# Performance work log

Hardware: AMD Instinct MI355X
Metric: run time of the kernel (lower is better)

Reference implementation:

```python
import jax, jax.numpy as jnp
import numpy as np


def setup_inputs() -> dict:
    key = jax.random.key(0)
    ks = jax.random.split(key, 8)
    B, T, D, H, R = 64, 1024, 512, 512, 64
    s = lambda n: 1.0 / np.sqrt(n)
    return {
        "x":   jax.random.normal(ks[0], (B, T, D), jnp.float32),
        "W_w": jax.random.normal(ks[1], (4 * H, D), jnp.float32) * s(D),
        "W_b": jax.random.normal(ks[2], (4 * H,), jnp.float32) * 0.01,
        "U_w": jax.random.normal(ks[3], (4 * H, H), jnp.float32) * s(H),
        "U_b": jax.random.normal(ks[4], (4 * H,), jnp.float32) * 0.01,
        "A_w": jax.random.normal(ks[5], (R, D), jnp.float32) * s(D),
        "B_w": jax.random.normal(ks[6], (R, H), jnp.float32) * s(H),
        "P_w": jax.random.normal(ks[7], (H, R), jnp.float32) * s(R),
    }


def reference(x, W_w, W_b, U_w, U_b, A_w, B_w, P_w):
    # x: [B,T,D]. Dropout is identity (eval mode).
    Bsz, T, _ = x.shape
    H = U_w.shape[0] // 4
    # Precompute all input-side projections in parallel (no recurrence dep).
    Wx = jnp.einsum('btd,hd->bth', x, W_w) + W_b          # [B,T,4H]
    Ax = jnp.einsum('btd,rd->btr', x, A_w)                # [B,T,R]

    def step(carry, inp):
        h, c = carry
        wx_t, ax_t = inp                                  # [B,4H], [B,R]
        gates = wx_t + h @ U_w.T + U_b                    # [B,4H]
        i, f, o, g = jnp.split(gates, 4, axis=-1)
        i = jax.nn.sigmoid(i)
        f = jax.nn.sigmoid(f)
        o = jax.nn.sigmoid(o)
        g = jnp.tanh(g)
        mix = (ax_t * (h @ B_w.T)) @ P_w.T                # [B,H]
        c = f * c + i * g + 0.1 * mix
        h = o * jnp.tanh(c)
        return (h, c), h

    h0 = jnp.zeros((Bsz, H), x.dtype)
    c0 = jnp.zeros((Bsz, H), x.dtype)
    (h, c), outs = jax.lax.scan(
        step, (h0, c0),
        (jnp.swapaxes(Wx, 0, 1), jnp.swapaxes(Ax, 0, 1)))
    outs = jnp.swapaxes(outs, 0, 1)                       # [B,T,H]
    return outs, h, c
```

## Files before the change

### kernel.cpp

```cpp
#include <hip/hip_runtime.h>
#include <stdint.h>


typedef float    f32x4  __attribute__((ext_vector_type(4)));
typedef __bf16   bf16x8 __attribute__((ext_vector_type(8)));
typedef uint16_t u16;
typedef uint16_t u16x8  __attribute__((ext_vector_type(8)));

#define WS_XB     0
#define WS_WC     67108864
#define WS_BIAS   69337088
#define WS_U      69345792
#define WS_BW     71442944
#define WS_P      71508480
#define WS_HBUF   71574016
#define WS_CNT    71705088
#define WS_WXC    71706112

#define OUT_H     33554432
#define OUT_C     33587200

#define SMEM_BYTES (16384 + 4352 + 4352 + 1088)

__device__ __forceinline__ u16 f2bf(float f) {
  uint32_t u = __builtin_bit_cast(uint32_t, f);
  u = (u + 0x7fffu + ((u >> 16) & 1u)) >> 16;
  return (u16)u;
}
__device__ __forceinline__ float bf2f(u16 b) {
  uint32_t u = ((uint32_t)b) << 16;
  return __builtin_bit_cast(float, u);
}
__device__ __forceinline__ f32x4 mfma16(u16x8 a, u16x8 b, f32x4 c) {
  return __builtin_amdgcn_mfma_f32_16x16x32_bf16(
      __builtin_bit_cast(bf16x8, a), __builtin_bit_cast(bf16x8, b), c, 0, 0, 0);
}
__device__ __forceinline__ float sigm(float x) { return 1.f / (1.f + __expf(-x)); }
__device__ __forceinline__ float tanh_fast(float x) {
  float a = fabsf(x);
  float e = __expf(2.f * a);
  float t = 1.f - 2.f / (e + 1.f);
  return x < 0.f ? -t : t;
}

__global__ void cast_x(const float* __restrict__ x, u16* __restrict__ xb) {
  int i = blockIdx.x * 256 + threadIdx.x;
  const float4* src = (const float4*)x;
  float4 a = src[(size_t)i * 2];
  float4 b = src[(size_t)i * 2 + 1];
  u16x8 o;
  o[0] = f2bf(a.x); o[1] = f2bf(a.y); o[2] = f2bf(a.z); o[3] = f2bf(a.w);
  o[4] = f2bf(b.x); o[5] = f2bf(b.y); o[6] = f2bf(b.z); o[7] = f2bf(b.w);
  *(u16x8*)(xb + (size_t)i * 8) = o;
}

__global__ void prep(const float* __restrict__ W_w, const float* __restrict__ W_b,
                     const float* __restrict__ U_w, const float* __restrict__ U_b,
                     const float* __restrict__ A_w, const float* __restrict__ B_w,
                     const float* __restrict__ P_w,
                     u16* __restrict__ Wc, float* __restrict__ bias,
                     u16* __restrict__ Ubf, u16* __restrict__ Bwbf,
                     u16* __restrict__ Pbf, int* __restrict__ cnt) {
  const int total = 1114112 + 1048576 + 32768 + 32768 + 2176 + 256;
  for (int i = blockIdx.x * blockDim.x + threadIdx.x; i < total;
       i += gridDim.x * blockDim.x) {
    int idx = i;
    if (idx < 1114112) {
      int row = idx >> 9, k = idx & 511;
      float v = 0.f;
      if (row < 2048) v = W_w[row * 512 + k];
      else if (row < 2112) v = A_w[(row - 2048) * 512 + k];
      Wc[idx] = f2bf(v);
      continue;
    }
    idx -= 1114112;
    if (idx < 1048576) { Ubf[idx] = f2bf(U_w[idx]); continue; }
    idx -= 1048576;
    if (idx < 32768) { Bwbf[idx] = f2bf(B_w[idx]); continue; }
    idx -= 32768;
    if (idx < 32768) { Pbf[idx] = f2bf(0.1f * P_w[idx]); continue; }
    idx -= 32768;
    if (idx < 2176) {
      bias[idx] = (idx < 2048) ? (W_b[idx] + U_b[idx]) : 0.f;
      continue;
    }
    idx -= 2176;
    cnt[idx] = 0;
  }
}

__global__ void __launch_bounds__(256) gemm_wxc(const u16* __restrict__ xb,
                                                const u16* __restrict__ Wc,
                                                const float* __restrict__ bias,
                                                u16* __restrict__ outWx) {
  __shared__ u16 Atile[128 * 64];
  __shared__ u16 Btile[128 * 64];
  const int n0 = blockIdx.x * 128;
  const int m0 = blockIdx.y * 128;
  const int tid = threadIdx.x, ln = tid & 63, wv = tid >> 6;
  const int wm = (wv >> 1) * 64, wn = (wv & 1) * 64;
  f32x4 acc[4][4] = {};

  for (int k0 = 0; k0 < 512; k0 += 64) {
    __syncthreads();
    #pragma unroll
    for (int q = 0; q < 4; ++q) {
      int idx = tid + q * 256;
      int row = idx >> 3, kc = idx & 7;
      uint4 va = *(const uint4*)(xb + (size_t)(m0 + row) * 512 + k0 + kc * 8);
      *(uint4*)((char*)Atile + row * 128 + ((kc * 16) ^ ((row & 7) << 4))) = va;
      uint4 vb = *(const uint4*)(Wc + (size_t)(n0 + row) * 512 + k0 + kc * 8);
      *(uint4*)((char*)Btile + row * 128 + ((kc * 16) ^ ((row & 7) << 4))) = vb;
    }
    __syncthreads();
    #pragma unroll
    for (int kk = 0; kk < 64; kk += 32) {
      u16x8 af[4], bf[4];
      const int kb = kk * 2 + ((ln >> 4) << 4);
      #pragma unroll
      for (int i = 0; i < 4; ++i) {
        int arow = wm + i * 16 + (ln & 15);
        af[i] = *(const u16x8*)((char*)Atile + arow * 128 + (kb ^ ((arow & 7) << 4)));
        int brow = wn + i * 16 + (ln & 15);
        bf[i] = *(const u16x8*)((char*)Btile + brow * 128 + (kb ^ ((brow & 7) << 4)));
      }
      #pragma unroll
      for (int i = 0; i < 4; ++i)
        #pragma unroll
        for (int j = 0; j < 4; ++j)
          acc[i][j] = mfma16(af[i], bf[j], acc[i][j]);
    }
  }
  #pragma unroll
  for (int i = 0; i < 4; ++i) {
    const int mrow = m0 + wm + i * 16 + ((ln >> 4) << 2);
    #pragma unroll
    for (int j = 0; j < 4; ++j) {
      const int n = n0 + wn + j * 16 + (ln & 15);
      if (n < 2112) {
        const float bv = bias[n];
        #pragma unroll
        for (int r = 0; r < 4; ++r)
          outWx[(size_t)(mrow + r) * 2112 + n] = f2bf(acc[i][j][r] + bv);
      }
    }
  }
}

__global__ void __launch_bounds__(512) recurrent(const u16* __restrict__ Wxc,
                                                 const u16* __restrict__ Ubf,
                                                 const u16* __restrict__ Bwbf,
                                                 const u16* __restrict__ Pbf,
                                                 u16* __restrict__ hbuf,
                                                 int* __restrict__ cnt,
                                                 float* __restrict__ out) {
  extern __shared__ char smem[];
  char*  h_lds   = smem;
  float* v_buf   = (float*)(smem + 16384);
  float* g_buf   = (float*)(smem + 16384 + 4352);
  float* mix_buf = (float*)(smem + 16384 + 4352 + 4352);

  const int tid = threadIdx.x;
  const int wv  = tid >> 6;
  const int ln  = tid & 63;
  const int grp = blockIdx.x & 3;
  const int ublk = blockIdx.x >> 2;
  const int u0 = ublk << 4;
  const int b0 = grp << 4;

  u16x8 bfrag[16];
  {
    const u16* src = (wv < 4)
        ? (Ubf + (size_t)(wv * 512 + u0 + (ln & 15)) * 512)
        : (Bwbf + (size_t)((wv - 4) * 16 + (ln & 15)) * 512);
    #pragma unroll
    for (int ks = 0; ks < 16; ++ks)
      bfrag[ks] = *(const u16x8*)(src + ks * 32 + ((ln >> 4) << 3));
  }
  u16x8 pfrag[2];
  #pragma unroll
  for (int ks = 0; ks < 2; ++ks)
    pfrag[ks] = *(const u16x8*)(Pbf + (size_t)(u0 + (ln & 15)) * 64 + ks * 32 + ((ln >> 4) << 3));

  for (int i = tid; i < 1024; i += 512) ((uint4*)h_lds)[i] = make_uint4(0, 0, 0, 0);

  const int arow_base = (ln & 15) * 1024;
  const int a_xor = (ln & 7) << 4;
  const int a_k0 = (ln >> 4) << 4;
  const int myb = tid >> 4, myu = tid & 15;
  float c_reg = 0.f, h_last = 0.f;

  __syncthreads();

  #pragma unroll 1
  for (int t = 0; t < 1024; ++t) {
    u16 wxu[4];
    if (wv < 4) {
      const int col = wv * 512 + u0 + (ln & 15);
      const size_t rb = ((size_t)(b0 + ((ln >> 4) << 2)) * 1024 + t) * 2112;
      #pragma unroll
      for (int j = 0; j < 4; ++j) wxu[j] = Wxc[rb + (size_t)j * 1024 * 2112 + col];
    }
    u16x8 axu0, axu1;
    if (wv == 0) {
      const u16* axp = Wxc + ((size_t)(b0 + (ln & 15)) * 1024 + t) * 2112 + 2048 + ((ln >> 4) << 3);
      axu0 = *(const u16x8*)(axp);
      axu1 = *(const u16x8*)(axp + 32);
    }

    f32x4 acc = {0.f, 0.f, 0.f, 0.f};
    #pragma unroll
    for (int ks = 0; ks < 16; ++ks) {
      const int kb = ks * 64 + a_k0;
      u16x8 afr = *(const u16x8*)(h_lds + arow_base + (kb ^ a_xor));
      acc = mfma16(afr, bfrag[ks], acc);
    }

    if (wv >= 4) {
      const int r = ((wv - 4) << 4) + (ln & 15);
      const int br = (ln >> 4) << 2;
      #pragma unroll
      for (int j = 0; j < 4; ++j) v_buf[(br + j) * 68 + r] = acc[j];
    } else {
      const int gi = wv * 272 + (ln & 15);
      const int br = (ln >> 4) << 2;
      #pragma unroll
      for (int j = 0; j < 4; ++j) {
        float g = acc[j] + bf2f(wxu[j]);
        g = (wv == 3) ? tanh_fast(g) : sigm(g);
        g_buf[gi + (br + j) * 17] = g;
      }
    }
    __syncthreads();

    if (wv == 0) {
      f32x4 accm = {0.f, 0.f, 0.f, 0.f};
      const int bb = ln & 15;
      const int r0 = (ln >> 4) << 3;
      u16x8 af;
      #pragma unroll
      for (int i = 0; i < 8; ++i)
        af[i] = f2bf(bf2f(axu0[i]) * v_buf[bb * 68 + r0 + i]);
      accm = mfma16(af, pfrag[0], accm);
      #pragma unroll
      for (int i = 0; i < 8; ++i)
        af[i] = f2bf(bf2f(axu1[i]) * v_buf[bb * 68 + 32 + r0 + i]);
      accm = mfma16(af, pfrag[1], accm);
      const int br = (ln >> 4) << 2;
      #pragma unroll
      for (int j = 0; j < 4; ++j) mix_buf[(br + j) * 17 + bb] = accm[j];
    }
    __syncthreads();

    if (tid < 256) {
      const int go = myb * 17 + myu;
      float iv = g_buf[go];
      float fv = g_buf[272 + go];
      float ov = g_buf[544 + go];
      float gv = g_buf[816 + go];
      float mx = mix_buf[go];
      c_reg = fv * c_reg + iv * gv + mx;
      float h = ov * tanh_fast(c_reg);
      h_last = h;
      out[((size_t)(b0 + myb) * 1024 + t) * 512 + u0 + myu] = h;
      __hip_atomic_store(hbuf + (size_t)(t & 1) * 32768 + (size_t)(b0 + myb) * 512 + u0 + myu,
                         f2bf(h), __ATOMIC_RELAXED, __HIP_MEMORY_SCOPE_AGENT);
    }

    asm volatile("s_waitcnt vmcnt(0)" ::: "memory");
    __syncthreads();
    if (tid == 0) {
      __hip_atomic_fetch_add(cnt + grp * 64, 1, __ATOMIC_RELAXED, __HIP_MEMORY_SCOPE_AGENT);
      const int target = 32 * (t + 1);
      while (__hip_atomic_load(cnt + grp * 64, __ATOMIC_RELAXED, __HIP_MEMORY_SCOPE_AGENT) < target) {}
    }
    __syncthreads();

    {
      const unsigned long long* src =
          (const unsigned long long*)(hbuf + (size_t)(t & 1) * 32768 + (size_t)b0 * 512);
      #pragma unroll
      for (int q = 0; q < 2; ++q) {
        int idx = tid + q * 512;
        int row = idx >> 6, kc = idx & 63;
        unsigned long long lo = __hip_atomic_load(src + (size_t)idx * 2,
                                                  __ATOMIC_RELAXED, __HIP_MEMORY_SCOPE_AGENT);
        unsigned long long hi = __hip_atomic_load(src + (size_t)idx * 2 + 1,
                                                  __ATOMIC_RELAXED, __HIP_MEMORY_SCOPE_AGENT);
        uint4 val;
        val.x = (uint32_t)lo; val.y = (uint32_t)(lo >> 32);
        val.z = (uint32_t)hi; val.w = (uint32_t)(hi >> 32);
        *(uint4*)(h_lds + row * 1024 + ((kc * 16) ^ ((row & 7) << 4))) = val;
      }
    }
    __syncthreads();
  }

  if (tid < 256) {
    out[OUT_H + (size_t)(b0 + myb) * 512 + u0 + myu] = h_last;
    out[OUT_C + (size_t)(b0 + myb) * 512 + u0 + myu] = c_reg;
  }
}

extern "C" void kernel_launch(void* const* d_in, const int* in_sizes, int n_in,
                              void* d_out, int out_size, void* d_ws, size_t ws_size,
                              hipStream_t stream) {
  const float* x   = (const float*)d_in[0];
  const float* W_w = (const float*)d_in[1];
  const float* W_b = (const float*)d_in[2];
  const float* U_w = (const float*)d_in[3];
  const float* U_b = (const float*)d_in[4];
  const float* A_w = (const float*)d_in[5];
  const float* B_w = (const float*)d_in[6];
  const float* P_w = (const float*)d_in[7];
  char* ws = (char*)d_ws;

  u16*   xb   = (u16*)(ws + WS_XB);
  u16*   Wc   = (u16*)(ws + WS_WC);
  float* bias = (float*)(ws + WS_BIAS);
  u16*   Ubf  = (u16*)(ws + WS_U);
  u16*   Bwbf = (u16*)(ws + WS_BW);
  u16*   Pbf  = (u16*)(ws + WS_P);
  u16*   hbuf = (u16*)(ws + WS_HBUF);
  int*   cnt  = (int*)(ws + WS_CNT);
  u16*   Wxc  = (u16*)(ws + WS_WXC);
  float* outp = (float*)d_out;

  cast_x<<<16384, 256, 0, stream>>>(x, xb);
  prep<<<2048, 256, 0, stream>>>(W_w, W_b, U_w, U_b, A_w, B_w, P_w,
                                 Wc, bias, Ubf, Bwbf, Pbf, cnt);
  gemm_wxc<<<dim3(17, 512), 256, 0, stream>>>(xb, Wc, bias, Wxc);

  void* args[] = { &Wxc, &Ubf, &Bwbf, &Pbf, &hbuf, &cnt, &outp };
  hipError_t e = hipLaunchCooperativeKernel((const void*)recurrent, dim3(128),
                                            dim3(512), args, SMEM_BYTES, stream);
  if (e != hipSuccess) {
    recurrent<<<dim3(128), dim3(512), SMEM_BYTES, stream>>>(Wxc, Ubf, Bwbf, Pbf,
                                                            hbuf, cnt, outp);
  }
}
```

Measured before the change: 3.996 ms.

## Split recurrent kernel into 8 batch groups with per-block flag barriers

The recurrent cooperative kernel now runs 256 blocks, each covering 8 batch rows instead of 16, which doubles parallelism across CUs. The single atomic-counter barrier is replaced by per-block step flags polled with a wave ballot, and the cell update plus h publish is folded into wave 0. That removes one __syncthreads and the mix buffer. Wx/Ax loads for step t+1 are prefetched while waiting on other blocks, and the MFMA chain is split into two accumulators. The trade-off is that half the MFMA rows are wasted padding and more blocks contend on global flags.

```diff
diff --git a/kernel.cpp b/kernel.cpp
--- a/kernel.cpp
+++ b/kernel.cpp
@@ -6,6 +6,7 @@
 typedef __bf16   bf16x8 __attribute__((ext_vector_type(8)));
 typedef uint16_t u16;
 typedef uint16_t u16x8  __attribute__((ext_vector_type(8)));
+typedef uint32_t u32x4  __attribute__((ext_vector_type(4)));
 
 #define WS_XB     0
 #define WS_WC     67108864
@@ -20,8 +21,6 @@
 #define OUT_H     33554432
 #define OUT_C     33587200
 
-#define SMEM_BYTES (16384 + 4352 + 4352 + 1088)
-
 __device__ __forceinline__ u16 f2bf(float f) {
   uint32_t u = __builtin_bit_cast(uint32_t, f);
   u = (u + 0x7fffu + ((u >> 16) & 1u)) >> 16;
@@ -60,7 +59,7 @@
                      const float* __restrict__ P_w,
                      u16* __restrict__ Wc, float* __restrict__ bias,
                      u16* __restrict__ Ubf, u16* __restrict__ Bwbf,
-                     u16* __restrict__ Pbf, int* __restrict__ cnt) {
+                     u16* __restrict__ Pbf, int* __restrict__ flags) {
   const int total = 1114112 + 1048576 + 32768 + 32768 + 2176 + 256;
   for (int i = blockIdx.x * blockDim.x + threadIdx.x; i < total;
        i += gridDim.x * blockDim.x) {
@@ -85,7 +84,7 @@
       continue;
     }
     idx -= 2176;
-    cnt[idx] = 0;
+    flags[idx] = 0;
   }
 }
 
@@ -147,26 +146,25 @@
   }
 }
 
-__global__ void __launch_bounds__(512) recurrent(const u16* __restrict__ Wxc,
-                                                 const u16* __restrict__ Ubf,
-                                                 const u16* __restrict__ Bwbf,
-                                                 const u16* __restrict__ Pbf,
-                                                 u16* __restrict__ hbuf,
-                                                 int* __restrict__ cnt,
-                                                 float* __restrict__ out) {
-  extern __shared__ char smem[];
-  char*  h_lds   = smem;
-  float* v_buf   = (float*)(smem + 16384);
-  float* g_buf   = (float*)(smem + 16384 + 4352);
-  float* mix_buf = (float*)(smem + 16384 + 4352 + 4352);
+__global__ void __launch_bounds__(512, 2) recurrent(const u16* __restrict__ Wxc,
+                                                    const u16* __restrict__ Ubf,
+                                                    const u16* __restrict__ Bwbf,
+                                                    const u16* __restrict__ Pbf,
+                                                    u16* __restrict__ hbuf,
+                                                    int* __restrict__ flagbuf,
+                                                    float* __restrict__ out) {
+  __shared__ char  h_lds[16 * 1024];
+  __shared__ float v_buf[16 * 68];
+  __shared__ float g_buf[4 * 8 * 17];
 
   const int tid = threadIdx.x;
-  const int wv  = tid >> 6;
-  const int ln  = tid & 63;
-  const int grp = blockIdx.x & 3;
-  const int ublk = blockIdx.x >> 2;
-  const int u0 = ublk << 4;
-  const int b0 = grp << 4;
+  const int wv = tid >> 6, ln = tid & 63;
+  const int grp = blockIdx.x & 7;
+  const int ublk = blockIdx.x >> 3;
+  const int u0 = ublk << 4, b0 = grp << 3;
+
+  int* flags  = flagbuf + grp * 32;
+  int* myflag = flags + ublk;
 
   u16x8 bfrag[16];
   {
@@ -182,51 +180,58 @@
   for (int ks = 0; ks < 2; ++ks)
     pfrag[ks] = *(const u16x8*)(Pbf + (size_t)(u0 + (ln & 15)) * 64 + ks * 32 + ((ln >> 4) << 3));
 
-  for (int i = tid; i < 1024; i += 512) ((uint4*)h_lds)[i] = make_uint4(0, 0, 0, 0);
+  for (int i = tid; i < 1024; i += 512)
+    ((u32x4*)h_lds)[i] = (u32x4){0u, 0u, 0u, 0u};
+  __syncthreads();
 
   const int arow_base = (ln & 15) * 1024;
   const int a_xor = (ln & 7) << 4;
   const int a_k0 = (ln >> 4) << 4;
-  const int myb = tid >> 4, myu = tid & 15;
-  float c_reg = 0.f, h_last = 0.f;
-
-  __syncthreads();
+
+  uint32_t wx_cur[4] = {0, 0, 0, 0};
+  u16x8 ax0_cur = {}, ax1_cur = {};
+  {
+    if (wv < 4 && ln < 32) {
+      const int col = wv * 512 + u0 + (ln & 15);
+      const size_t rb = ((size_t)(b0 + ((ln >> 4) << 2)) * 1024 + 0) * 2112;
+      #pragma unroll
+      for (int j = 0; j < 4; ++j) wx_cur[j] = Wxc[rb + (size_t)j * 1024 * 2112 + col];
+    }
+    if (wv == 0) {
+      const int bb = ln & 15;
+      const int bc = bb < 8 ? bb : 7;
+      const u16* axp = Wxc + ((size_t)(b0 + bc) * 1024 + 0) * 2112 + 2048 + ((ln >> 4) << 3);
+      ax0_cur = *(const u16x8*)(axp);
+      ax1_cur = *(const u16x8*)(axp + 32);
+    }
+  }
+
+  float c_reg[4] = {0.f, 0.f, 0.f, 0.f};
+  float h_last[4] = {0.f, 0.f, 0.f, 0.f};
 
   #pragma unroll 1
   for (int t = 0; t < 1024; ++t) {
-    u16 wxu[4];
-    if (wv < 4) {
-      const int col = wv * 512 + u0 + (ln & 15);
-      const size_t rb = ((size_t)(b0 + ((ln >> 4) << 2)) * 1024 + t) * 2112;
-      #pragma unroll
-      for (int j = 0; j < 4; ++j) wxu[j] = Wxc[rb + (size_t)j * 1024 * 2112 + col];
-    }
-    u16x8 axu0, axu1;
-    if (wv == 0) {
-      const u16* axp = Wxc + ((size_t)(b0 + (ln & 15)) * 1024 + t) * 2112 + 2048 + ((ln >> 4) << 3);
-      axu0 = *(const u16x8*)(axp);
-      axu1 = *(const u16x8*)(axp + 32);
-    }
-
-    f32x4 acc = {0.f, 0.f, 0.f, 0.f};
-    #pragma unroll
-    for (int ks = 0; ks < 16; ++ks) {
-      const int kb = ks * 64 + a_k0;
-      u16x8 afr = *(const u16x8*)(h_lds + arow_base + (kb ^ a_xor));
-      acc = mfma16(afr, bfrag[ks], acc);
-    }
+    f32x4 acc0 = {0.f, 0.f, 0.f, 0.f}, acc1 = {0.f, 0.f, 0.f, 0.f};
+    #pragma unroll
+    for (int ks = 0; ks < 16; ks += 2) {
+      u16x8 a0 = *(const u16x8*)(h_lds + arow_base + ((ks * 64 + a_k0) ^ a_xor));
+      u16x8 a1 = *(const u16x8*)(h_lds + arow_base + (((ks + 1) * 64 + a_k0) ^ a_xor));
+      acc0 = mfma16(a0, bfrag[ks], acc0);
+      acc1 = mfma16(a1, bfrag[ks + 1], acc1);
+    }
+    const f32x4 acc = acc0 + acc1;
 
     if (wv >= 4) {
       const int r = ((wv - 4) << 4) + (ln & 15);
       const int br = (ln >> 4) << 2;
       #pragma unroll
       for (int j = 0; j < 4; ++j) v_buf[(br + j) * 68 + r] = acc[j];
-    } else {
-      const int gi = wv * 272 + (ln & 15);
+    } else if (ln < 32) {
+      const int gi = wv * 136 + (ln & 15);
       const int br = (ln >> 4) << 2;
       #pragma unroll
       for (int j = 0; j < 4; ++j) {
-        float g = acc[j] + bf2f(wxu[j]);
+        float g = acc[j] + bf2f((u16)wx_cur[j]);
         g = (wv == 3) ? tanh_fast(g) : sigm(g);
         g_buf[gi + (br + j) * 17] = g;
       }
@@ -240,65 +245,91 @@
       u16x8 af;
       #pragma unroll
       for (int i = 0; i < 8; ++i)
-        af[i] = f2bf(bf2f(axu0[i]) * v_buf[bb * 68 + r0 + i]);
+        af[i] = f2bf(bf2f(ax0_cur[i]) * v_buf[bb * 68 + r0 + i]);
       accm = mfma16(af, pfrag[0], accm);
       #pragma unroll
       for (int i = 0; i < 8; ++i)
-        af[i] = f2bf(bf2f(axu1[i]) * v_buf[bb * 68 + 32 + r0 + i]);
+        af[i] = f2bf(bf2f(ax1_cur[i]) * v_buf[bb * 68 + 32 + r0 + i]);
       accm = mfma16(af, pfrag[1], accm);
-      const int br = (ln >> 4) << 2;
-      #pragma unroll
-      for (int j = 0; j < 4; ++j) mix_buf[(br + j) * 17 + bb] = accm[j];
+      float hv[4];
+      if (ln < 32) {
+        const int u = ln & 15;
+        const int brb = (ln >> 4) * 4;
+        u16* hdst = hbuf + (size_t)(t & 1) * 32768;
+        #pragma unroll
+        for (int j = 0; j < 4; ++j) {
+          const int go = (brb + j) * 17 + u;
+          float iv = g_buf[go];
+          float fv = g_buf[136 + go];
+          float ov = g_buf[272 + go];
+          float gv = g_buf[408 + go];
+          c_reg[j] = fv * c_reg[j] + iv * gv + accm[j];
+          hv[j] = ov * tanh_fast(c_reg[j]);
+          h_last[j] = hv[j];
+          __hip_atomic_store(hdst + (size_t)(b0 + brb + j) * 512 + u0 + u,
+                             f2bf(hv[j]), __ATOMIC_RELAXED, __HIP_MEMORY_SCOPE_AGENT);
+        }
+      }
+      asm volatile("s_waitcnt vmcnt(0)" ::: "memory");
+      if (ln == 0)
+        __hip_atomic_store(myflag, t + 1, __ATOMIC_RELAXED, __HIP_MEMORY_SCOPE_AGENT);
+      if (ln < 32) {
+        const int u = ln & 15;
+        const int brb = (ln >> 4) * 4;
+        #pragma unroll
+        for (int j = 0; j < 4; ++j)
+          out[((size_t)(b0 + brb + j) * 1024 + t) * 512 + u0 + u] = hv[j];
+      }
+    }
+
+    {
+      int* fp = flags + (ln & 31);
+      const int target = t + 1;
+      while (true) {
+        int f = __hip_atomic_load(fp, __ATOMIC_RELAXED, __HIP_MEMORY_SCOPE_AGENT);
+        if (__ballot(f >= target) == ~0ull) break;
+      }
+      asm volatile("" ::: "memory");
+    }
+
+    {
+      const int tn = (t < 1023) ? t + 1 : 1023;
+      if (wv < 4 && ln < 32) {
+        const int col = wv * 512 + u0 + (ln & 15);
+        const size_t rb = ((size_t)(b0 + ((ln >> 4) << 2)) * 1024 + tn) * 2112;
+        #pragma unroll
+        for (int j = 0; j < 4; ++j) wx_cur[j] = Wxc[rb + (size_t)j * 1024 * 2112 + col];
+      }
+      if (wv == 0) {
+        const int bb = ln & 15;
+        const int bc = bb < 8 ? bb : 7;
+        const u16* axp = Wxc + ((size_t)(b0 + bc) * 1024 + tn) * 2112 + 2048 + ((ln >> 4) << 3);
+        ax0_cur = *(const u16x8*)(axp);
+        ax1_cur = *(const u16x8*)(axp + 32);
+      }
+    }
+
+    {
+      const int row = tid >> 6, kc = tid & 63;
+      const unsigned long long* src = (const unsigned long long*)
+          (hbuf + (size_t)(t & 1) * 32768 + (size_t)(b0 + row) * 512 + kc * 8);
+      unsigned long long lo = __hip_atomic_load(src, __ATOMIC_RELAXED, __HIP_MEMORY_SCOPE_AGENT);
+      unsigned long long hi = __hip_atomic_load(src + 1, __ATOMIC_RELAXED, __HIP_MEMORY_SCOPE_AGENT);
+      uint4 val;
+      val.x = (uint32_t)lo; val.y = (uint32_t)(lo >> 32);
+      val.z = (uint32_t)hi; val.w = (uint32_t)(hi >> 32);
+      *(uint4*)(h_lds + row * 1024 + ((kc * 16) ^ ((row & 7) << 4))) = val;
     }
     __syncthreads();
-
-    if (tid < 256) {
-      const int go = myb * 17 + myu;
-      float iv = g_buf[go];
-      float fv = g_buf[272 + go];
-      float ov = g_buf[544 + go];
-      float gv = g_buf[816 + go];
-      float mx = mix_buf[go];
-      c_reg = fv * c_reg + iv * gv + mx;
-      float h = ov * tanh_fast(c_reg);
-      h_last = h;
-      out[((size_t)(b0 + myb) * 1024 + t) * 512 + u0 + myu] = h;
-      __hip_atomic_store(hbuf + (size_t)(t & 1) * 32768 + (size_t)(b0 + myb) * 512 + u0 + myu,
-                         f2bf(h), __ATOMIC_RELAXED, __HIP_MEMORY_SCOPE_AGENT);
-    }
-
-    asm volatile("s_waitcnt vmcnt(0)" ::: "memory");
-    __syncthreads();
-    if (tid == 0) {
-      __hip_atomic_fetch_add(cnt + grp * 64, 1, __ATOMIC_RELAXED, __HIP_MEMORY_SCOPE_AGENT);
-      const int target = 32 * (t + 1);
-      while (__hip_atomic_load(cnt + grp * 64, __ATOMIC_RELAXED, __HIP_MEMORY_SCOPE_AGENT) < target) {}
-    }
-    __syncthreads();
-
-    {
-      const unsigned long long* src =
-          (const unsigned long long*)(hbuf + (size_t)(t & 1) * 32768 + (size_t)b0 * 512);
-      #pragma unroll
-      for (int q = 0; q < 2; ++q) {
-        int idx = tid + q * 512;
-        int row = idx >> 6, kc = idx & 63;
-        unsigned long long lo = __hip_atomic_load(src + (size_t)idx * 2,
-                                                  __ATOMIC_RELAXED, __HIP_MEMORY_SCOPE_AGENT);
-        unsigned long long hi = __hip_atomic_load(src + (size_t)idx * 2 + 1,
-                                                  __ATOMIC_RELAXED, __HIP_MEMORY_SCOPE_AGENT);
-        uint4 val;
-        val.x = (uint32_t)lo; val.y = (uint32_t)(lo >> 32);
-        val.z = (uint32_t)hi; val.w = (uint32_t)(hi >> 32);
-        *(uint4*)(h_lds + row * 1024 + ((kc * 16) ^ ((row & 7) << 4))) = val;
-      }
-    }
-    __syncthreads();
-  }
-
-  if (tid < 256) {
-    out[OUT_H + (size_t)(b0 + myb) * 512 + u0 + myu] = h_last;
-    out[OUT_C + (size_t)(b0 + myb) * 512 + u0 + myu] = c_reg;
+  }
+
+  if (wv == 0 && ln < 32) {
+    const int u = ln & 15, brb = (ln >> 4) * 4;
+    #pragma unroll
+    for (int j = 0; j < 4; ++j) {
+      out[OUT_H + (size_t)(b0 + brb + j) * 512 + u0 + u] = h_last[j];
+      out[OUT_C + (size_t)(b0 + brb + j) * 512 + u0 + u] = c_reg[j];
+    }
   }
 }
 
@@ -322,20 +353,20 @@
   u16*   Bwbf = (u16*)(ws + WS_BW);
   u16*   Pbf  = (u16*)(ws + WS_P);
   u16*   hbuf = (u16*)(ws + WS_HBUF);
-  int*   cnt  = (int*)(ws + WS_CNT);
+  int*   flg  = (int*)(ws + WS_CNT);
   u16*   Wxc  = (u16*)(ws + WS_WXC);
   float* outp = (float*)d_out;
 
   cast_x<<<16384, 256, 0, stream>>>(x, xb);
   prep<<<2048, 256, 0, stream>>>(W_w, W_b, U_w, U_b, A_w, B_w, P_w,
-                                 Wc, bias, Ubf, Bwbf, Pbf, cnt);
+                                 Wc, bias, Ubf, Bwbf, Pbf, flg);
   gemm_wxc<<<dim3(17, 512), 256, 0, stream>>>(xb, Wc, bias, Wxc);
 
-  void* args[] = { &Wxc, &Ubf, &Bwbf, &Pbf, &hbuf, &cnt, &outp };
-  hipError_t e = hipLaunchCooperativeKernel((const void*)recurrent, dim3(128),
-                                            dim3(512), args, SMEM_BYTES, stream);
+  void* args[] = { &Wxc, &Ubf, &Bwbf, &Pbf, &hbuf, &flg, &outp };
+  hipError_t e = hipLaunchCooperativeKernel((const void*)recurrent, dim3(256),
+                                            dim3(512), args, 0, stream);
   if (e != hipSuccess) {
-    recurrent<<<dim3(128), dim3(512), SMEM_BYTES, stream>>>(Wxc, Ubf, Bwbf, Pbf,
-                                                            hbuf, cnt, outp);
-  }
-}
+    recurrent<<<dim3(256), dim3(512), 0, stream>>>(Wxc, Ubf, Bwbf, Pbf,
+                                                   hbuf, flg, outp);
+  }
+}
```

New measurement: 7.939 ms. +98.7%, slower.
